# Performance work log

Hardware: AMD Instinct MI355X
Metric: run time of the kernel (lower is better)

Reference implementation:

```python
import jax, jax.numpy as jnp
import numpy as np

FLT_BACKWARP = 2.5  # Matching.fltBackwarp for intLevel == 4
NEG_SLOPE = 0.1


def backwarp(ten_input, ten_flow):
    # torch grid_sample(mode='bilinear', padding_mode='zeros', align_corners=True)
    # with grid = base + flow*2/(size-1) is equivalent to sampling at pixel coords
    # (x + u, y + v) with zero padding outside [0, W-1] x [0, H-1].
    B, C, H, W = ten_input.shape
    xs = jnp.arange(W, dtype=ten_input.dtype)
    ys = jnp.arange(H, dtype=ten_input.dtype)
    px = xs[None, None, :] + ten_flow[:, 0]  # [B,H,W]
    py = ys[None, :, None] + ten_flow[:, 1]  # [B,H,W]
    x0 = jnp.floor(px)
    y0 = jnp.floor(py)
    x1 = x0 + 1.0
    y1 = y0 + 1.0
    wx1 = px - x0
    wx0 = 1.0 - wx1
    wy1 = py - y0
    wy0 = 1.0 - wy1

    def gather(ix, iy):
        valid = ((ix >= 0) & (ix <= W - 1) & (iy >= 0) & (iy <= H - 1)).astype(ten_input.dtype)
        ixc = jnp.clip(ix, 0, W - 1).astype(jnp.int32)
        iyc = jnp.clip(iy, 0, H - 1).astype(jnp.int32)
        v = jax.vmap(lambda img, yy, xx: img[:, yy, xx])(ten_input, iyc, ixc)  # [B,C,H,W]
        return v * valid[:, None]

    return (gather(x0, y0) * (wx0 * wy0)[:, None]
            + gather(x1, y0) * (wx1 * wy0)[:, None]
            + gather(x0, y1) * (wx0 * wy1)[:, None]
            + gather(x1, y1) * (wx1 * wy1)[:, None])


def correlation(one, two, stride):
    # FunctionCorrelation: 7x7 displacement window, offsets (-3..3)*stride,
    # zero pad 3*stride, dot over channels / C. Output [B,49,ceil(H/s),ceil(W/s)].
    B, C, H, W = one.shape
    p = 3 * stride
    two_pad = jnp.pad(two, ((0, 0), (0, 0), (p, p), (p, p)))
    one_s = one[:, :, ::stride, ::stride]  # [B,C,Ho,Wo]
    outs = []
    for dj in range(-3, 4):  # channel index k = (dj+3)*7 + (di+3)
        for di in range(-3, 4):
            y0 = p + dj * stride
            x0 = p + di * stride
            shift = two_pad[:, :, y0:y0 + H:stride, x0:x0 + W:stride]
            outs.append(jnp.einsum('bchw,bchw->bhw', one_s, shift))
    return jnp.stack(outs, axis=1) / jnp.asarray(C, one.dtype)


def setup_inputs() -> dict:
    key = jax.random.key(0)
    k1, k2, k3 = jax.random.split(key, 3)
    B, C, H, W = 2, 128, 256, 448
    return {
        'tenOne': jax.random.normal(k1, (B, C, H, W), dtype=jnp.float32),
        'tenTwo': jax.random.normal(k2, (B, C, H, W), dtype=jnp.float32),
        'tenFlow': jax.random.normal(k3, (B, 2, H, W), dtype=jnp.float32),
        'intStride': 1,
    }


def reference(tenOne, tenTwo, tenFlow, intStride):
    warped = backwarp(tenTwo, tenFlow * FLT_BACKWARP)
    corr = correlation(tenOne, warped, int(intStride))
    return jax.nn.leaky_relu(corr, NEG_SLOPE)
```

## Files before the change

kernel.cpp:

```cpp
#include <hip/hip_runtime.h>
#include <hip/hip_bf16.h>

#define BB 2
#define CC 128
#define HH 256
#define WW 448
#define KK 49
#define HWSZ (HH * WW)
#define PW 456

#define WT_BYTES ((size_t)BB * HH * PW * CC * 2)
#define TWT_BYTES ((size_t)BB * HH * WW * CC * 2)
#define WS_NEED (WT_BYTES + TWT_BYTES)

typedef __attribute__((ext_vector_type(8))) short bf16x8;
typedef __attribute__((ext_vector_type(4))) float f32x4;
typedef __attribute__((ext_vector_type(8))) unsigned short u16x8;

static __device__ __forceinline__ short f2bf(float v) {
  __hip_bfloat16 h = __float2bfloat16(v);
  return *reinterpret_cast<short*>(&h);
}
static __device__ __forceinline__ float bf2f(unsigned short u) {
  unsigned int x = ((unsigned int)u) << 16;
  return __uint_as_float(x);
}

typedef const __attribute__((address_space(1))) unsigned int* as1_u32p;
typedef __attribute__((address_space(3))) unsigned int* as3_u32p;
static __device__ __forceinline__ void gload_lds16(const void* g, void* l) {
  __builtin_amdgcn_global_load_lds((as1_u32p)g, (as3_u32p)l, 16, 0, 0);
}

__global__ __launch_bounds__(256) void border_kernel(__hip_bfloat16* wt) {
  int i = blockIdx.x * 256 + threadIdx.x;
  int by = i >> 7;
  int r = i & 127;
  int ps = r >> 4;
  int c16 = r & 15;
  int px = (ps < 4) ? ps : (448 + ps);
  u16x8 z = {0, 0, 0, 0, 0, 0, 0, 0};
  *(u16x8*)((char*)wt + ((size_t)((size_t)by * PW + px) * CC + c16 * 8) * 2) = z;
}

__global__ __launch_bounds__(256) void transpose_kernel(
    const float* __restrict__ two, __hip_bfloat16* __restrict__ two_t) {
  __shared__ float lds[128 * 33];
  int bid = blockIdx.x;
  int b = bid / (HWSZ / 32);
  int tile = bid - b * (HWSZ / 32);
  int P0 = tile * 32;

  const float* src = two + (size_t)b * CC * HWSZ + P0;
  int t = threadIdx.x;
  int bc = t >> 3;
  int f = t & 7;
#pragma unroll
  for (int k = 0; k < 4; ++k) {
    int c = bc + k * 32;
    float4 v = *(const float4*)(src + (size_t)c * HWSZ + f * 4);
    float* d = &lds[c * 33 + f * 4];
    d[0] = v.x; d[1] = v.y; d[2] = v.z; d[3] = v.w;
  }
  __syncthreads();

  int q = t & 7;
  int pl = t >> 3;
  int cs = q * 16;
  u16x8 pk0, pk1;
#pragma unroll
  for (int j = 0; j < 8; ++j)
    pk0[j] = (unsigned short)f2bf(lds[(cs + j) * 33 + pl]);
#pragma unroll
  for (int j = 0; j < 8; ++j)
    pk1[j] = (unsigned short)f2bf(lds[(cs + 8 + j) * 33 + pl]);
  char* dst = (char*)two_t + ((size_t)((size_t)b * HWSZ + P0 + pl) * CC + cs) * 2;
  *(u16x8*)dst = pk0;
  *(u16x8*)(dst + 16) = pk1;
}

__global__ __launch_bounds__(256) void warp_fast(
    const __hip_bfloat16* __restrict__ two_t, const float* __restrict__ flow,
    __hip_bfloat16* __restrict__ wt) {
  int wg = (blockIdx.x & 7) * 128 + (blockIdx.x >> 3);
  int b = wg >> 9;
  int rem = wg & 511;
  int y = rem >> 1;
  int X0 = (rem & 1) * 224;
  int pg = threadIdx.x >> 4;
  int cw = threadIdx.x & 15;

  const char* tb = (const char*)two_t + (size_t)b * HWSZ * (CC * 2);
  char* wb = (char*)wt + ((size_t)(b * HH + y) * PW + 4) * (CC * 2);
  const float* fxp = flow + (size_t)(b * 2 + 0) * HWSZ + y * WW;
  const float* fyp = flow + (size_t)(b * 2 + 1) * HWSZ + y * WW;

#pragma unroll 2
  for (int it = 0; it < 14; ++it) {
    int x = X0 + it * 16 + pg;

    float fx = fxp[x] * 2.5f;
    float fy = fyp[x] * 2.5f;
    float px = (float)x + fx;
    float py = (float)y + fy;
    float x0f = floorf(px), y0f = floorf(py);
    int x0 = (int)x0f, y0 = (int)y0f;
    int x1 = x0 + 1, y1 = y0 + 1;
    float wx1 = px - x0f, wx0 = 1.0f - wx1;
    float wy1 = py - y0f, wy0 = 1.0f - wy1;
    bool vx0 = (x0 >= 0) && (x0 < WW);
    bool vx1 = (x1 >= 0) && (x1 < WW);
    bool vy0 = (y0 >= 0) && (y0 < HH);
    bool vy1 = (y1 >= 0) && (y1 < HH);
    float w00 = (vx0 && vy0) ? wx0 * wy0 : 0.0f;
    float w01 = (vx1 && vy0) ? wx1 * wy0 : 0.0f;
    float w10 = (vx0 && vy1) ? wx0 * wy1 : 0.0f;
    float w11 = (vx1 && vy1) ? wx1 * wy1 : 0.0f;
    int cx0 = min(max(x0, 0), WW - 1);
    int cx1 = min(max(x1, 0), WW - 1);
    int cy0 = min(max(y0, 0), HH - 1);
    int cy1 = min(max(y1, 0), HH - 1);

    u16x8 a = *(const u16x8*)(tb + ((size_t)cy0 * WW + cx0) * 256 + cw * 16);
    u16x8 bb_ = *(const u16x8*)(tb + ((size_t)cy0 * WW + cx1) * 256 + cw * 16);
    u16x8 c = *(const u16x8*)(tb + ((size_t)cy1 * WW + cx0) * 256 + cw * 16);
    u16x8 d = *(const u16x8*)(tb + ((size_t)cy1 * WW + cx1) * 256 + cw * 16);

    u16x8 pk;
#pragma unroll
    for (int e = 0; e < 8; ++e) {
      float v = w00 * bf2f((unsigned short)a[e]) +
                w01 * bf2f((unsigned short)bb_[e]) +
                w10 * bf2f((unsigned short)c[e]) +
                w11 * bf2f((unsigned short)d[e]);
      pk[e] = (unsigned short)f2bf(v);
    }
    *(u16x8*)(wb + (size_t)x * 256 + cw * 16) = pk;
  }
}

__global__ __launch_bounds__(256) void warp_fallback(
    const float* __restrict__ two, const float* __restrict__ flow,
    __hip_bfloat16* __restrict__ wt) {
  int idx = blockIdx.x * 256 + threadIdx.x;
  if (idx >= BB * HWSZ) return;
  int x = idx % WW;
  int y = (idx / WW) % HH;
  int b = idx / HWSZ;

  float fx = flow[(b * 2 + 0) * HWSZ + y * WW + x] * 2.5f;
  float fy = flow[(b * 2 + 1) * HWSZ + y * WW + x] * 2.5f;
  float px = (float)x + fx;
  float py = (float)y + fy;
  float x0f = floorf(px), y0f = floorf(py);
  int x0 = (int)x0f, y0 = (int)y0f;
  int x1 = x0 + 1, y1 = y0 + 1;
  float wx1 = px - x0f, wx0 = 1.0f - wx1;
  float wy1 = py - y0f, wy0 = 1.0f - wy1;
  bool vx0 = (x0 >= 0) && (x0 < WW);
  bool vx1 = (x1 >= 0) && (x1 < WW);
  bool vy0 = (y0 >= 0) && (y0 < HH);
  bool vy1 = (y1 >= 0) && (y1 < HH);
  float w00 = (vx0 && vy0) ? wx0 * wy0 : 0.0f;
  float w01 = (vx1 && vy0) ? wx1 * wy0 : 0.0f;
  float w10 = (vx0 && vy1) ? wx0 * wy1 : 0.0f;
  float w11 = (vx1 && vy1) ? wx1 * wy1 : 0.0f;
  int cx0 = min(max(x0, 0), WW - 1);
  int cx1 = min(max(x1, 0), WW - 1);
  int cy0 = min(max(y0, 0), HH - 1);
  int cy1 = min(max(y1, 0), HH - 1);
  int o00 = cy0 * WW + cx0;
  int o01 = cy0 * WW + cx1;
  int o10 = cy1 * WW + cx0;
  int o11 = cy1 * WW + cx1;

  const float* p = two + (size_t)b * CC * HWSZ;
  char* wo = (char*)wt + ((size_t)((size_t)(b * HH + y) * PW) + x + 4) * CC * 2;
#pragma unroll 4
  for (int j = 0; j < 16; ++j) {
    u16x8 pk;
#pragma unroll
    for (int jj = 0; jj < 8; ++jj) {
      int c = j * 8 + jj;
      const float* pc = p + (size_t)c * HWSZ;
      float v = w00 * pc[o00] + w01 * pc[o01] + w10 * pc[o10] + w11 * pc[o11];
      pk[jj] = (unsigned short)f2bf(v);
    }
    *(u16x8*)(wo + j * 16) = pk;
  }
}

#define YTB 8
#define NROWS 14
#define NPOS 22
#define ROWCH (NPOS * 16)
#define CHUNKS (NROWS * ROWCH)

__global__ __launch_bounds__(512, 4) void corr_kernel(
    const float* __restrict__ one, const __hip_bfloat16* __restrict__ wt,
    float* __restrict__ out) {
  __shared__ uint4 ldsb[CHUNKS];

  int bid = blockIdx.x;
  int wg = (bid & 7) * 224 + (bid >> 3);
  int b = wg / 896;
  int rem = wg - b * 896;
  int xt = rem >> 5;
  int yt = rem & 31;
  int ybase = yt * YTB;
  int X0 = xt * 16;
  int tid = threadIdx.x;
  int w = tid >> 6;
  int l = tid & 63;
  int lp = l & 15;
  int lg = l >> 4;
  int y = ybase + w;

  const char* wbase =
      (const char*)wt + (((size_t)(b * HH)) * PW + X0 + 1) * (CC * 2);
  bool interior = (ybase >= 3) && (ybase + NROWS - 3 <= HH);

  if (interior) {
#pragma unroll
    for (int k = 0; k < 10; ++k) {
      int ci = tid + k * 512;
      if (k < 9 || tid < (CHUNKS - 9 * 512)) {
        int row = ci / ROWCH;
        int r2 = ci - row * ROWCH;
        int p = r2 >> 4;
        int cw = r2 & 15;
        int cwS = cw ^ (p & 7);
        int yy = ybase - 3 + row;
        const char* g = wbase + (size_t)yy * (PW * CC * 2) + p * 256 + cwS * 16;
        int wave_ci0 = k * 512 + (tid & ~63);
        gload_lds16(g, (char*)ldsb + (size_t)wave_ci0 * 16);
      }
    }
  } else {
#pragma unroll
    for (int k = 0; k < 10; ++k) {
      int ci = tid + k * 512;
      if (ci < CHUNKS) {
        int row = ci / ROWCH;
        int r2 = ci - row * ROWCH;
        int p = r2 >> 4;
        int cw = r2 & 15;
        int yy = ybase - 3 + row;
        uint4 v = {0, 0, 0, 0};
        if (yy >= 0 && yy < HH)
          v = *(const uint4*)(wbase + (size_t)yy * (PW * CC * 2) + p * 256 +
                              cw * 16);
        *(uint4*)((char*)ldsb + ((ci * 16) ^ ((p & 7) << 4))) = v;
      }
    }
  }

  const float* Abase = one + ((size_t)(b * CC) * HH + y) * WW + X0 + lp;
  bf16x8 afr[4];
#pragma unroll
  for (int t = 0; t < 4; ++t)
#pragma unroll
    for (int j = 0; j < 8; ++j)
      afr[t][j] = f2bf(Abase[(size_t)(t * 32 + lg * 8 + j) * HWSZ]);

  __syncthreads();

  int p1 = (lp + 16 < 21) ? (lp + 16) : 21;
  int cosw0[4], cosw1[4];
#pragma unroll
  for (int t = 0; t < 4; ++t) {
    int co = t * 64 + lg * 16;
    cosw0[t] = co ^ ((lp & 7) << 4);
    cosw1[t] = co ^ ((p1 & 7) << 4);
  }

  f32x4 acc[7][2] = {};
#pragma unroll
  for (int dj = 0; dj < 7; ++dj) {
    int rl = w + dj;
    int b0 = (rl * NPOS + lp) << 8;
    int b1 = (rl * NPOS + p1) << 8;
#pragma unroll
    for (int t = 0; t < 4; ++t) {
      bf16x8 v0 = *(const bf16x8*)((const char*)ldsb + (b0 + cosw0[t]));
      bf16x8 v1 = *(const bf16x8*)((const char*)ldsb + (b1 + cosw1[t]));
      acc[dj][0] = __builtin_amdgcn_mfma_f32_16x16x32_bf16(afr[t], v0,
                                                           acc[dj][0], 0, 0, 0);
      acc[dj][1] = __builtin_amdgcn_mfma_f32_16x16x32_bf16(afr[t], v1,
                                                           acc[dj][1], 0, 0, 0);
    }
  }

  __syncthreads();
  float* sc = (float*)ldsb;
#pragma unroll
  for (int dj = 0; dj < 7; ++dj) {
#pragma unroll
    for (int nt = 0; nt < 2; ++nt) {
      int post = lp + 16 * nt;
#pragma unroll
      for (int r = 0; r < 4; ++r) {
        int xlc = 4 * lg + r;
        int di = post - xlc;
        if (di >= 0 && di <= 6) {
          int k = dj * 7 + di;
          sc[k * 128 + w * 16 + ((xlc + k) & 15)] = acc[dj][nt][r];
        }
      }
    }
  }
  __syncthreads();

  float* ob = out + (size_t)(b * KK) * HWSZ + (size_t)ybase * WW + X0;
#pragma unroll
  for (int i = 0; i < 13; ++i) {
    int e = tid + i * 512;
    if (e < KK * 128) {
      int k = e >> 7;
      int yr = (e >> 4) & 7;
      int px = e & 15;
      float v = sc[k * 128 + yr * 16 + ((px + k) & 15)] * (1.0f / 128.0f);
      v = (v > 0.0f) ? v : 0.1f * v;
      ob[(size_t)k * HWSZ + yr * WW + px] = v;
    }
  }
}

extern "C" void kernel_launch(void* const* d_in, const int* in_sizes, int n_in,
                              void* d_out, int out_size, void* d_ws,
                              size_t ws_size, hipStream_t stream) {
  const float* tenOne = (const float*)d_in[0];
  const float* tenTwo = (const float*)d_in[1];
  const float* tenFlow = (const float*)d_in[2];

  __hip_bfloat16* wt = (__hip_bfloat16*)d_ws;
  border_kernel<<<256, 256, 0, stream>>>(wt);

  if (ws_size >= WS_NEED) {
    __hip_bfloat16* two_t = (__hip_bfloat16*)((char*)d_ws + WT_BYTES);
    transpose_kernel<<<BB * (HWSZ / 32), 256, 0, stream>>>(tenTwo, two_t);
    warp_fast<<<1024, 256, 0, stream>>>(two_t, tenFlow, wt);
  } else {
    int blocks = (BB * HWSZ + 255) / 256;
    warp_fallback<<<blocks, 256, 0, stream>>>(tenTwo, tenFlow, wt);
  }
  corr_kernel<<<1792, 512, 0, stream>>>(tenOne, wt, (float*)d_out);
}
```

Before: 136.2 us.

## Make corr kernel persistent with double-buffered LDS staging and prefetched A loads

The correlation kernel becomes persistent: 256 blocks each loop over 7 tiles. While one tile is computed, the next tile's warped-feature window is staged into a second LDS buffer with async global-to-LDS loads, and its tenOne fragments are prefetched into registers. This is meant to hide load latency behind the MFMA work. Border handling changes from a separate non-interior path to zero-filling only the out-of-range rows. The warp kernel is also reshaped to one 1024-thread block per image row. The costs are double LDS use, fewer resident blocks per CU (256 blocks on a 256-CU part), higher register pressure from the 64-float prefetch buffers, and a dropped occupancy hint.

```diff
diff --git a/kernel.cpp b/kernel.cpp
--- a/kernel.cpp
+++ b/kernel.cpp
@@ -79,14 +79,12 @@
   *(u16x8*)(dst + 16) = pk1;
 }
 
-__global__ __launch_bounds__(256) void warp_fast(
+__global__ __launch_bounds__(1024) void warp_fast(
     const __hip_bfloat16* __restrict__ two_t, const float* __restrict__ flow,
     __hip_bfloat16* __restrict__ wt) {
-  int wg = (blockIdx.x & 7) * 128 + (blockIdx.x >> 3);
-  int b = wg >> 9;
-  int rem = wg & 511;
-  int y = rem >> 1;
-  int X0 = (rem & 1) * 224;
+  int wg = (blockIdx.x & 7) * 64 + (blockIdx.x >> 3);
+  int b = wg >> 8;
+  int y = wg & 255;
   int pg = threadIdx.x >> 4;
   int cw = threadIdx.x & 15;
 
@@ -96,8 +94,8 @@
   const float* fyp = flow + (size_t)(b * 2 + 1) * HWSZ + y * WW;
 
 #pragma unroll 2
-  for (int it = 0; it < 14; ++it) {
-    int x = X0 + it * 16 + pg;
+  for (int it = 0; it < 7; ++it) {
+    int x = it * 64 + pg;
 
     float fx = fxp[x] * 2.5f;
     float fy = fyp[x] * 2.5f;
@@ -196,75 +194,30 @@
 #define ROWCH (NPOS * 16)
 #define CHUNKS (NROWS * ROWCH)
 
-__global__ __launch_bounds__(512, 4) void corr_kernel(
+__global__ __launch_bounds__(512) void corr_kernel(
     const float* __restrict__ one, const __hip_bfloat16* __restrict__ wt,
     float* __restrict__ out) {
-  __shared__ uint4 ldsb[CHUNKS];
+  __shared__ uint4 ldsb[2][CHUNKS];
 
   int bid = blockIdx.x;
-  int wg = (bid & 7) * 224 + (bid >> 3);
-  int b = wg / 896;
-  int rem = wg - b * 896;
-  int xt = rem >> 5;
-  int yt = rem & 31;
-  int ybase = yt * YTB;
-  int X0 = xt * 16;
   int tid = threadIdx.x;
   int w = tid >> 6;
   int l = tid & 63;
   int lp = l & 15;
   int lg = l >> 4;
-  int y = ybase + w;
-
-  const char* wbase =
-      (const char*)wt + (((size_t)(b * HH)) * PW + X0 + 1) * (CC * 2);
-  bool interior = (ybase >= 3) && (ybase + NROWS - 3 <= HH);
-
-  if (interior) {
-#pragma unroll
-    for (int k = 0; k < 10; ++k) {
-      int ci = tid + k * 512;
-      if (k < 9 || tid < (CHUNKS - 9 * 512)) {
-        int row = ci / ROWCH;
-        int r2 = ci - row * ROWCH;
-        int p = r2 >> 4;
-        int cw = r2 & 15;
-        int cwS = cw ^ (p & 7);
-        int yy = ybase - 3 + row;
-        const char* g = wbase + (size_t)yy * (PW * CC * 2) + p * 256 + cwS * 16;
-        int wave_ci0 = k * 512 + (tid & ~63);
-        gload_lds16(g, (char*)ldsb + (size_t)wave_ci0 * 16);
-      }
-    }
-  } else {
-#pragma unroll
-    for (int k = 0; k < 10; ++k) {
-      int ci = tid + k * 512;
-      if (ci < CHUNKS) {
-        int row = ci / ROWCH;
-        int r2 = ci - row * ROWCH;
-        int p = r2 >> 4;
-        int cw = r2 & 15;
-        int yy = ybase - 3 + row;
-        uint4 v = {0, 0, 0, 0};
-        if (yy >= 0 && yy < HH)
-          v = *(const uint4*)(wbase + (size_t)yy * (PW * CC * 2) + p * 256 +
-                              cw * 16);
-        *(uint4*)((char*)ldsb + ((ci * 16) ^ ((p & 7) << 4))) = v;
-      }
-    }
-  }
-
-  const float* Abase = one + ((size_t)(b * CC) * HH + y) * WW + X0 + lp;
-  bf16x8 afr[4];
-#pragma unroll
-  for (int t = 0; t < 4; ++t)
-#pragma unroll
-    for (int j = 0; j < 8; ++j)
-      afr[t][j] = f2bf(Abase[(size_t)(t * 32 + lg * 8 + j) * HWSZ]);
-
-  __syncthreads();
-
+
+  int srow[10], soff[10];
+#pragma unroll
+  for (int k = 0; k < 10; ++k) {
+    int ci = tid + k * 512;
+    int row = ci / ROWCH;
+    int r2 = ci - row * ROWCH;
+    int p = r2 >> 4;
+    int cw = r2 & 15;
+    int cwS = cw ^ (p & 7);
+    srow[k] = row;
+    soff[k] = row * (PW * CC * 2) + p * 256 + cwS * 16;
+  }
   int p1 = (lp + 16 < 21) ? (lp + 16) : 21;
   int cosw0[4], cosw1[4];
 #pragma unroll
@@ -274,54 +227,134 @@
     cosw1[t] = co ^ ((p1 & 7) << 4);
   }
 
-  f32x4 acc[7][2] = {};
-#pragma unroll
-  for (int dj = 0; dj < 7; ++dj) {
-    int rl = w + dj;
-    int b0 = (rl * NPOS + lp) << 8;
-    int b1 = (rl * NPOS + p1) << 8;
-#pragma unroll
-    for (int t = 0; t < 4; ++t) {
-      bf16x8 v0 = *(const bf16x8*)((const char*)ldsb + (b0 + cosw0[t]));
-      bf16x8 v1 = *(const bf16x8*)((const char*)ldsb + (b1 + cosw1[t]));
-      acc[dj][0] = __builtin_amdgcn_mfma_f32_16x16x32_bf16(afr[t], v0,
-                                                           acc[dj][0], 0, 0, 0);
-      acc[dj][1] = __builtin_amdgcn_mfma_f32_16x16x32_bf16(afr[t], v1,
-                                                           acc[dj][1], 0, 0, 0);
-    }
-  }
-
-  __syncthreads();
-  float* sc = (float*)ldsb;
-#pragma unroll
-  for (int dj = 0; dj < 7; ++dj) {
-#pragma unroll
-    for (int nt = 0; nt < 2; ++nt) {
-      int post = lp + 16 * nt;
-#pragma unroll
-      for (int r = 0; r < 4; ++r) {
-        int xlc = 4 * lg + r;
-        int di = post - xlc;
-        if (di >= 0 && di <= 6) {
-          int k = dj * 7 + di;
-          sc[k * 128 + w * 16 + ((xlc + k) & 15)] = acc[dj][nt][r];
+  uint4 zz = {0, 0, 0, 0};
+  auto stage = [&](int t, uint4* buf) {
+    int b = t / 896;
+    int rem = t - b * 896;
+    int xt = rem >> 5;
+    int yt = rem & 31;
+    int ybase = yt * YTB;
+    int X0 = xt * 16;
+    const char* wbase =
+        (const char*)wt + (((size_t)(b * HH)) * PW + X0 + 1) * (CC * 2);
+    const char* gb = wbase + (ptrdiff_t)(ybase - 3) * (PW * CC * 2);
+    if (yt == 0) {
+#pragma unroll
+      for (int k2 = 0; k2 < 3; ++k2) {
+        int ci = tid + k2 * 512;
+        if (ci < 3 * ROWCH) buf[ci] = zz;
+      }
+    } else if (yt == 31) {
+#pragma unroll
+      for (int k2 = 0; k2 < 3; ++k2) {
+        int ci = tid + k2 * 512;
+        if (ci < 3 * ROWCH) buf[11 * ROWCH + ci] = zz;
+      }
+    }
+#pragma unroll
+    for (int k = 0; k < 10; ++k) {
+      bool inb = (k < 9) || (tid < (CHUNKS - 9 * 512));
+      unsigned yy = (unsigned)(ybase - 3 + srow[k]);
+      if (inb && yy < HH)
+        gload_lds16(gb + soff[k],
+                    (char*)buf + (size_t)(k * 512 + (tid & ~63)) * 16);
+    }
+  };
+  auto aload = [&](int t, float* af) {
+    int b = t / 896;
+    int rem = t - b * 896;
+    int xt = rem >> 5;
+    int yt = rem & 31;
+    int y = yt * YTB + w;
+    int X0 = xt * 16;
+    const float* Ab = one + ((size_t)(b * CC) * HH + y) * WW + X0 + lp;
+#pragma unroll
+    for (int tt = 0; tt < 4; ++tt)
+#pragma unroll
+      for (int j = 0; j < 8; ++j)
+        af[tt * 8 + j] = Ab[(size_t)(tt * 32 + lg * 8 + j) * HWSZ];
+  };
+
+  float af0[32], af1[32];
+  stage(bid, ldsb[0]);
+  aload(bid, af0);
+
+#pragma unroll
+  for (int i = 0; i < 7; ++i) {
+    const int cur = i & 1;
+    int t = i * 256 + bid;
+    int b = t / 896;
+    int rem = t - b * 896;
+    int xt = rem >> 5;
+    int yt = rem & 31;
+    int ybase = yt * YTB;
+    int X0 = xt * 16;
+
+    __syncthreads();
+
+    if (i + 1 < 7) {
+      stage((i + 1) * 256 + bid, ldsb[cur ^ 1]);
+      if ((i + 1) & 1) aload((i + 1) * 256 + bid, af1);
+      else             aload((i + 1) * 256 + bid, af0);
+    }
+
+    float* afc = (i & 1) ? af1 : af0;
+    bf16x8 afr[4];
+#pragma unroll
+    for (int tt = 0; tt < 4; ++tt)
+#pragma unroll
+      for (int j = 0; j < 8; ++j) afr[tt][j] = f2bf(afc[tt * 8 + j]);
+
+    const char* bufc = (const char*)ldsb[cur];
+    f32x4 acc[7][2] = {};
+#pragma unroll
+    for (int dj = 0; dj < 7; ++dj) {
+      int rl = w + dj;
+      int b0 = (rl * NPOS + lp) << 8;
+      int b1 = (rl * NPOS + p1) << 8;
+#pragma unroll
+      for (int tt = 0; tt < 4; ++tt) {
+        bf16x8 v0 = *(const bf16x8*)(bufc + (b0 + cosw0[tt]));
+        bf16x8 v1 = *(const bf16x8*)(bufc + (b1 + cosw1[tt]));
+        acc[dj][0] = __builtin_amdgcn_mfma_f32_16x16x32_bf16(afr[tt], v0,
+                                                             acc[dj][0], 0, 0, 0);
+        acc[dj][1] = __builtin_amdgcn_mfma_f32_16x16x32_bf16(afr[tt], v1,
+                                                             acc[dj][1], 0, 0, 0);
+      }
+    }
+
+    __syncthreads();
+    float* sc = (float*)ldsb[cur];
+#pragma unroll
+    for (int dj = 0; dj < 7; ++dj) {
+#pragma unroll
+      for (int nt = 0; nt < 2; ++nt) {
+        int post = lp + 16 * nt;
+#pragma unroll
+        for (int r = 0; r < 4; ++r) {
+          int xlc = 4 * lg + r;
+          int di = post - xlc;
+          if (di >= 0 && di <= 6) {
+            int k = dj * 7 + di;
+            sc[k * 128 + w * 16 + ((xlc + k) & 15)] = acc[dj][nt][r];
+          }
         }
       }
     }
-  }
-  __syncthreads();
-
-  float* ob = out + (size_t)(b * KK) * HWSZ + (size_t)ybase * WW + X0;
-#pragma unroll
-  for (int i = 0; i < 13; ++i) {
-    int e = tid + i * 512;
-    if (e < KK * 128) {
-      int k = e >> 7;
-      int yr = (e >> 4) & 7;
-      int px = e & 15;
-      float v = sc[k * 128 + yr * 16 + ((px + k) & 15)] * (1.0f / 128.0f);
-      v = (v > 0.0f) ? v : 0.1f * v;
-      ob[(size_t)k * HWSZ + yr * WW + px] = v;
+    __syncthreads();
+
+    float* ob = out + (size_t)(b * KK) * HWSZ + (size_t)ybase * WW + X0;
+#pragma unroll
+    for (int ii = 0; ii < 13; ++ii) {
+      int e = tid + ii * 512;
+      if (e < KK * 128) {
+        int k = e >> 7;
+        int yr = (e >> 4) & 7;
+        int px = e & 15;
+        float v = sc[k * 128 + yr * 16 + ((px + k) & 15)] * (1.0f / 128.0f);
+        v = (v > 0.0f) ? v : 0.1f * v;
+        ob[(size_t)k * HWSZ + yr * WW + px] = v;
+      }
     }
   }
 }
@@ -339,10 +372,10 @@
   if (ws_size >= WS_NEED) {
     __hip_bfloat16* two_t = (__hip_bfloat16*)((char*)d_ws + WT_BYTES);
     transpose_kernel<<<BB * (HWSZ / 32), 256, 0, stream>>>(tenTwo, two_t);
-    warp_fast<<<1024, 256, 0, stream>>>(two_t, tenFlow, wt);
+    warp_fast<<<512, 1024, 0, stream>>>(two_t, tenFlow, wt);
   } else {
     int blocks = (BB * HWSZ + 255) / 256;
     warp_fallback<<<blocks, 256, 0, stream>>>(tenTwo, tenFlow, wt);
   }
-  corr_kernel<<<1792, 512, 0, stream>>>(tenOne, wt, (float*)d_out);
-}
+  corr_kernel<<<256, 512, 0, stream>>>(tenOne, wt, (float*)d_out);
+}
```

Result: slower. 244.1 us (+79.2%).
